# Performance work log

Measured on AMD Instinct MI355X. Metric: run time of the kernel, lower is better.

Reference implementation:

```python
import jax, jax.numpy as jnp
import numpy as np

B, T, I, H = 32768, 18, 2, 64  # batch, seq_len (forced by fc2 in_features=18), input_dim, hidden_dim


def setup_inputs() -> dict:
    key = jax.random.key(0)
    ks = jax.random.split(key, 13)
    s = 1.0 / np.sqrt(H)  # torch default GRU/Linear init scale
    return {
        "x": jax.random.normal(ks[0], (B, T, I), jnp.float32),
        "w_ih_f": jax.random.uniform(ks[1], (3 * H, I), jnp.float32, -s, s),
        "w_hh_f": jax.random.uniform(ks[2], (3 * H, H), jnp.float32, -s, s),
        "b_ih_f": jax.random.uniform(ks[3], (3 * H,), jnp.float32, -s, s),
        "b_hh_f": jax.random.uniform(ks[4], (3 * H,), jnp.float32, -s, s),
        "w_ih_b": jax.random.uniform(ks[5], (3 * H, I), jnp.float32, -s, s),
        "w_hh_b": jax.random.uniform(ks[6], (3 * H, H), jnp.float32, -s, s),
        "b_ih_b": jax.random.uniform(ks[7], (3 * H,), jnp.float32, -s, s),
        "b_hh_b": jax.random.uniform(ks[8], (3 * H,), jnp.float32, -s, s),
        "fc1_w": jax.random.uniform(ks[9], (24, 2 * H), jnp.float32, -s, s),
        "fc1_b": jax.random.uniform(ks[10], (24,), jnp.float32, -s, s),
        "fc2_w": jax.random.uniform(ks[11], (2, T), jnp.float32, -s, s),
        "fc2_b": jax.random.uniform(ks[12], (2,), jnp.float32, -s, s),
    }


def _gru_scan(x_proj, w_hh, b_hh):
    """x_proj: (T, B, 3H) precomputed input projections. Returns (T, B, H)."""
    h0 = jnp.zeros((x_proj.shape[1], w_hh.shape[1]), x_proj.dtype)

    def step(h, xp):
        gh = h @ w_hh.T + b_hh
        i_r, i_z, i_n = jnp.split(xp, 3, axis=-1)
        h_r, h_z, h_n = jnp.split(gh, 3, axis=-1)
        r = jax.nn.sigmoid(i_r + h_r)
        z = jax.nn.sigmoid(i_z + h_z)
        n = jnp.tanh(i_n + r * h_n)
        h_new = (1 - z) * n + z * h
        return h_new, h_new

    _, hs = jax.lax.scan(step, h0, x_proj)
    return hs


def reference(x, w_ih_f, w_hh_f, b_ih_f, b_hh_f,
              w_ih_b, w_hh_b, b_ih_b, b_hh_b,
              fc1_w, fc1_b, fc2_w, fc2_b):
    # precompute input-gate projections for both directions: (T, B, 3H)
    xp_f = jnp.einsum('bti,gi->tbg', x, w_ih_f) + b_ih_f
    xp_b = jnp.einsum('bti,gi->tbg', x[:, ::-1], w_ih_b) + b_ih_b
    hf = _gru_scan(xp_f, w_hh_f, b_hh_f)           # (T, B, H)
    hb = _gru_scan(xp_b, w_hh_b, b_hh_b)[::-1]     # (T, B, H), re-aligned to forward time
    out = jnp.concatenate([hf, hb], axis=-1).transpose(1, 0, 2)  # (B, T, 2H)
    out = out @ fc1_w.T + fc1_b                    # (B, T, 24)
    out = out.reshape(out.shape[0], 24, -1)        # (B, 24, T) raw row-major reshape, as in torch
    out = out @ fc2_w.T + fc2_b                    # (B, 24, 2)
    return out
```

## Files before the change

### kernel.cpp

```cpp
#include <hip/hip_runtime.h>

#define TT 18

typedef __attribute__((ext_vector_type(8))) short short8;
typedef __attribute__((ext_vector_type(4))) float float4_t;
typedef __attribute__((ext_vector_type(2))) float float2_t;
typedef __attribute__((ext_vector_type(2))) unsigned int uint2_t;

#if defined(__has_builtin)
#if __has_builtin(__builtin_amdgcn_exp2f)
#define FEXP2(x) __builtin_amdgcn_exp2f(x)
#else
#define FEXP2(x) exp2f(x)
#endif
#else
#define FEXP2(x) exp2f(x)
#endif

static __device__ __forceinline__ float frcp(float x){ return __builtin_amdgcn_rcpf(x); }
static __device__ __forceinline__ unsigned rne_bits(float f){
    unsigned u = __float_as_uint(f);
    return u + 0x7fffu + ((u >> 16) & 1u);
}
static __device__ __forceinline__ void bsplit(float f, unsigned &hi, unsigned &lo){
    unsigned rb = rne_bits(f);
    hi = rb >> 16;
    float fh = __uint_as_float(rb & 0xffff0000u);
    lo = rne_bits(f - fh) >> 16;
}
static __device__ __forceinline__ unsigned pack_hi16(unsigned hi_src, unsigned lo_src){
#if defined(__has_builtin)
#if __has_builtin(__builtin_amdgcn_perm)
    return __builtin_amdgcn_perm(hi_src, lo_src, 0x07060302u);
#else
    return (lo_src >> 16) | (hi_src & 0xffff0000u);
#endif
#else
    return (lo_src >> 16) | (hi_src & 0xffff0000u);
#endif
}

union U8 { short8 s; unsigned u[4]; };

#define MFMA16(A,B,C) __builtin_amdgcn_mfma_f32_16x16x32_bf16((A),(B),(C),0,0,0)

static __device__ __forceinline__ short8 make_b2f(float x0, float x1, bool q0){
    unsigned h0, l0, h1, l1;
    bsplit(x0, h0, l0);
    bsplit(x1, h1, l1);
    U8 B;
    B.u[0] = q0 ? (h0 | (l0 << 16)) : 0u;
    B.u[1] = q0 ? (h0 | (h1 << 16)) : 0u;
    B.u[2] = q0 ? (l1 | (h1 << 16)) : 0u;
    B.u[3] = q0 ? 0x3F803F80u : 0u;
    return B.s;
}

__global__ __launch_bounds__(256) void head_precompute(
    const float* __restrict__ fc1_w, const float* __restrict__ fc1_b,
    const float* __restrict__ fc2_w, const float* __restrict__ fc2_b,
    unsigned short* __restrict__ Bhi, unsigned short* __restrict__ Blo,
    float* __restrict__ Cvec)
{
    int idx = blockIdx.x * 256 + threadIdx.x;
    if (idx < 24 * 2 * 18 * 128) {
        int jg = idx & 127;
        int t  = (idx >> 7) % 18;
        int k  = (idx / 2304) & 1;
        int r  = idx / 4608;
        float acc = 0.f;
        for (int c = 0; c < 24; ++c) {
            int s = t * 24 + c - r * 18;
            if (s >= 0 && s < 18) acc += fc2_w[k * 18 + s] * fc1_w[c * 128 + jg];
        }
        unsigned hi, lo;
        bsplit(acc, hi, lo);
        Bhi[idx] = (unsigned short)hi;
        Blo[idx] = (unsigned short)lo;
    }
    if (idx < 48) {
        int k = idx & 1, r = idx >> 1;
        float acc = fc2_b[k];
        for (int s = 0; s < 18; ++s)
            acc += fc2_w[k * 18 + s] * fc1_b[(r * 18 + s) % 24];
        Cvec[idx] = acc;
    }
}

struct SMv {
    alignas(16) unsigned short hb[2][2][2][2048];
    float2_t x_s[32][18];
    float out_acc[2][32][49];
};

__global__ __launch_bounds__(512, 4) void gru_mfma(
    const float* __restrict__ x,
    const float* __restrict__ w_ih_f, const float* __restrict__ w_hh_f,
    const float* __restrict__ b_ih_f, const float* __restrict__ b_hh_f,
    const float* __restrict__ w_ih_b, const float* __restrict__ w_hh_b,
    const float* __restrict__ b_ih_b, const float* __restrict__ b_hh_b,
    const unsigned short* __restrict__ Bhi, const unsigned short* __restrict__ Blo,
    const float* __restrict__ Cvec, float* __restrict__ out)
{
    __shared__ SMv sm;
    const int tid  = threadIdx.x;
    const int lane = tid & 63;
    const int wave = tid >> 6;
    const int dir  = wave >> 2;
    const int jq   = wave & 3;
    const int col  = lane & 15;
    const int quad = lane >> 4;
    const int bb   = blockIdx.x * 32;
    const bool q0  = (quad == 0);

    const float* __restrict__ wih = dir ? w_ih_b : w_ih_f;
    const float* __restrict__ whh = dir ? w_hh_b : w_hh_f;
    const float* __restrict__ bih = dir ? b_ih_b : b_ih_f;
    const float* __restrict__ bhh = dir ? b_hh_b : b_hh_f;

    const float L1 = 1.4426950408889634f;
    const float L2 = 2.8853900817779268f;

    {
        unsigned* z = (unsigned*)&sm.hb[1][0][0][0];
        #pragma unroll
        for (int o = 0; o < 8; ++o) z[tid + o * 512] = 0u;
    }
    for (int o = tid; o < 2 * 32 * 49; o += 512) ((float*)sm.out_acc)[o] = 0.f;

    for (int p = tid; p < 32 * 18; p += 512) {
        int b = p / 18, t = p % 18;
        sm.x_s[b][t] = *(const float2_t*)(x + (size_t)(bb + b) * 36 + t * 2);
    }

    short8 wf[3][2];
    #pragma unroll
    for (int ty = 0; ty < 3; ++ty) {
        float sc = (ty == 2) ? L2 : L1;
        int g = ty * 64 + jq * 16 + col;
        #pragma unroll
        for (int c = 0; c < 2; ++c) {
            const float* p = whh + g * 64 + c * 32 + quad * 8;
            float4_t f0 = *(const float4_t*)p;
            float4_t f1 = *(const float4_t*)(p + 4);
            short8 s;
            #pragma unroll
            for (int e = 0; e < 8; ++e) {
                float f = (e < 4) ? f0[e] : f1[e - 4];
                s[e] = (short)(rne_bits(sc * f) >> 16);
            }
            wf[ty][c] = s;
        }
    }

    short8 c2[4];
    {
        int g0 = jq * 16 + col;
        #pragma unroll
        for (int ty = 0; ty < 2; ++ty) {
            int g = ty * 64 + g0;
            unsigned w0h, w0l, w1h, w1l, bh, bl;
            bsplit(L1 * wih[2 * g],     w0h, w0l);
            bsplit(L1 * wih[2 * g + 1], w1h, w1l);
            bsplit(L1 * (bih[g] + bhh[g]), bh, bl);
            U8 f;
            f.u[0] = q0 ? (w0h | (w0h << 16)) : 0u;
            f.u[1] = q0 ? (w0l | (w1h << 16)) : 0u;
            f.u[2] = q0 ? (w1h | (w1l << 16)) : 0u;
            f.u[3] = q0 ? (bh  | (bl  << 16)) : 0u;
            c2[ty] = f.s;
        }
        {
            unsigned bh, bl;
            bsplit(L2 * bhh[128 + g0], bh, bl);
            U8 f;
            f.u[0] = 0u; f.u[1] = 0u; f.u[2] = 0u;
            f.u[3] = q0 ? (bh | (bl << 16)) : 0u;
            c2[2] = f.s;
        }
        {
            int g = 128 + g0;
            unsigned w0h, w0l, w1h, w1l, bh, bl;
            bsplit(L2 * wih[2 * g],     w0h, w0l);
            bsplit(L2 * wih[2 * g + 1], w1h, w1l);
            bsplit(L2 * bih[g], bh, bl);
            U8 f;
            f.u[0] = q0 ? (w0h | (w0h << 16)) : 0u;
            f.u[1] = q0 ? (w0l | (w1h << 16)) : 0u;
            f.u[2] = q0 ? (w1h | (w1l << 16)) : 0u;
            f.u[3] = q0 ? (bh  | (bl  << 16)) : 0u;
            c2[3] = f.s;
        }
    }

    float hprev[8] = {0.f,0.f,0.f,0.f,0.f,0.f,0.f,0.f};

    __syncthreads();

    auto step = [&](int t, int pr, int pw) {
        const bool myturn = (t > 0) && (((t - 1) & 3) == jq);
        const int tx = dir ? (TT - 1 - t) : t;

        short8 h0c0 = *(const short8*)&sm.hb[pr][dir][0][quad * 256 + col * 8];
        short8 h0c1 = *(const short8*)&sm.hb[pr][dir][0][(4 + quad) * 256 + col * 8];
        short8 h1c0 = *(const short8*)&sm.hb[pr][dir][0][quad * 256 + (16 + col) * 8];
        short8 h1c1 = *(const short8*)&sm.hb[pr][dir][0][(4 + quad) * 256 + (16 + col) * 8];

        float2_t xv0 = sm.x_s[col][tx];
        float2_t xv1 = sm.x_s[16 + col][tx];
        short8 b2f0 = make_b2f(xv0[0], xv0[1], q0);
        short8 b2f1 = make_b2f(xv1[0], xv1[1], q0);

        short8 hA0, hA1, lA0, lA1, l0c0, l0c1, l1c0, l1c1;
        int base_h = 0;
        if (myturn) {
            int s  = t - 1;
            int ta = dir ? (TT - 1 - s) : s;
            base_h = 4 * (ta / 3) + ta % 3;
            int i  = col & 3;
            int rr = base_h + (i >> 1);
            int kk = i & 1;
            size_t boff = (size_t)((rr * 2 + kk) * TT + ta) * 128 + dir * 64 + quad * 8;
            hA0 = *(const short8*)(Bhi + boff);
            hA1 = *(const short8*)(Bhi + boff + 32);
            lA0 = *(const short8*)(Blo + boff);
            lA1 = *(const short8*)(Blo + boff + 32);
            l0c0 = *(const short8*)&sm.hb[pr][dir][1][quad * 256 + col * 8];
            l0c1 = *(const short8*)&sm.hb[pr][dir][1][(4 + quad) * 256 + col * 8];
            l1c0 = *(const short8*)&sm.hb[pr][dir][1][quad * 256 + (16 + col) * 8];
            l1c1 = *(const short8*)&sm.hb[pr][dir][1][(4 + quad) * 256 + (16 + col) * 8];
        }

        #pragma unroll
        for (int nt = 0; nt < 2; ++nt) {
            short8 hc0 = nt ? h1c0 : h0c0;
            short8 hc1 = nt ? h1c1 : h0c1;
            short8 b2f = nt ? b2f1 : b2f0;
            float4_t aR  = (float4_t){0.f,0.f,0.f,0.f};
            float4_t aZ  = (float4_t){0.f,0.f,0.f,0.f};
            float4_t aNH = (float4_t){0.f,0.f,0.f,0.f};
            float4_t aNX = (float4_t){0.f,0.f,0.f,0.f};
            aR  = MFMA16(wf[0][0], hc0, aR);
            aR  = MFMA16(wf[0][1], hc1, aR);
            aR  = MFMA16(c2[0],    b2f, aR);
            aZ  = MFMA16(wf[1][0], hc0, aZ);
            aZ  = MFMA16(wf[1][1], hc1, aZ);
            aZ  = MFMA16(c2[1],    b2f, aZ);
            aNH = MFMA16(wf[2][0], hc0, aNH);
            aNH = MFMA16(wf[2][1], hc1, aNH);
            aNH = MFMA16(c2[2],    b2f, aNH);
            aNX = MFMA16(c2[3],    b2f, aNX);

            unsigned rh[4], rl[4];
            #pragma unroll
            for (int reg = 0; reg < 4; ++reg) {
                float r = frcp(1.f + FEXP2(-aR[reg]));
                float z = frcp(1.f + FEXP2(-aZ[reg]));
                float a = fmaf(r, aNH[reg], aNX[reg]);
                float n = fmaf(2.f, frcp(1.f + FEXP2(-a)), -1.f);
                float hnew = fmaf(z, hprev[nt * 4 + reg] - n, n);
                hprev[nt * 4 + reg] = hnew;
                unsigned rb = rne_bits(hnew);
                rh[reg] = rb;
                rl[reg] = __float_as_uint(hnew - __uint_as_float(rb & 0xffff0000u));
            }
            int woff = (jq * 2 + (quad >> 1)) * 256 + (nt * 16 + col) * 8 + (quad & 1) * 4;
            uint2_t dh, dl;
            dh[0] = pack_hi16(rh[1], rh[0]);
            dh[1] = pack_hi16(rh[3], rh[2]);
            dl[0] = pack_hi16(rl[1], rl[0]);
            dl[1] = pack_hi16(rl[3], rl[2]);
            *(uint2_t*)&sm.hb[pw][dir][0][woff] = dh;
            *(uint2_t*)&sm.hb[pw][dir][1][woff] = dl;

            if (nt == 0 && myturn) {
                float4_t a0 = (float4_t){0.f,0.f,0.f,0.f};
                a0 = MFMA16(hA0, h0c0, a0);
                a0 = MFMA16(hA1, h0c1, a0);
                a0 = MFMA16(hA0, l0c0, a0);
                a0 = MFMA16(hA1, l0c1, a0);
                a0 = MFMA16(lA0, h0c0, a0);
                a0 = MFMA16(lA1, h0c1, a0);
                float4_t a1 = (float4_t){0.f,0.f,0.f,0.f};
                a1 = MFMA16(hA0, h1c0, a1);
                a1 = MFMA16(hA1, h1c1, a1);
                a1 = MFMA16(hA0, l1c0, a1);
                a1 = MFMA16(hA1, l1c1, a1);
                a1 = MFMA16(lA0, h1c0, a1);
                a1 = MFMA16(lA1, h1c1, a1);
                if (q0) {
                    #pragma unroll
                    for (int reg = 0; reg < 4; ++reg) {
                        int cell = (base_h + (reg >> 1)) * 2 + (reg & 1);
                        sm.out_acc[dir][col][cell]      += a0[reg];
                        sm.out_acc[dir][16 + col][cell] += a1[reg];
                    }
                }
            }
        }

        __syncthreads();
    };

    #pragma unroll 1
    for (int tt = 0; tt < 9; ++tt) {
        step(2 * tt,     1, 0);
        step(2 * tt + 1, 0, 1);
    }

    if (jq == ((TT - 1) & 3)) {
        int s  = TT - 1;
        int ta = dir ? 0 : s;
        int base_h = 4 * (ta / 3) + ta % 3;
        int i  = col & 3;
        int rr = base_h + (i >> 1);
        int kk = i & 1;
        size_t boff = (size_t)((rr * 2 + kk) * TT + ta) * 128 + dir * 64 + quad * 8;
        short8 hA0 = *(const short8*)(Bhi + boff);
        short8 hA1 = *(const short8*)(Bhi + boff + 32);
        short8 lA0 = *(const short8*)(Blo + boff);
        short8 lA1 = *(const short8*)(Blo + boff + 32);
        #pragma unroll
        for (int nt = 0; nt < 2; ++nt) {
            short8 hc0 = *(const short8*)&sm.hb[1][dir][0][quad * 256 + (nt * 16 + col) * 8];
            short8 hc1 = *(const short8*)&sm.hb[1][dir][0][(4 + quad) * 256 + (nt * 16 + col) * 8];
            short8 lc0 = *(const short8*)&sm.hb[1][dir][1][quad * 256 + (nt * 16 + col) * 8];
            short8 lc1 = *(const short8*)&sm.hb[1][dir][1][(4 + quad) * 256 + (nt * 16 + col) * 8];
            float4_t acch = (float4_t){0.f,0.f,0.f,0.f};
            acch = MFMA16(hA0, hc0, acch);
            acch = MFMA16(hA1, hc1, acch);
            acch = MFMA16(hA0, lc0, acch);
            acch = MFMA16(hA1, lc1, acch);
            acch = MFMA16(lA0, hc0, acch);
            acch = MFMA16(lA1, hc1, acch);
            if (q0) {
                #pragma unroll
                for (int reg = 0; reg < 4; ++reg) {
                    int cell = (base_h + (reg >> 1)) * 2 + (reg & 1);
                    sm.out_acc[dir][nt * 16 + col][cell] += acch[reg];
                }
            }
        }
    }
    __syncthreads();

    #pragma unroll
    for (int rep = 0; rep < 3; ++rep) {
        int o = rep * 512 + tid;
        int b = o / 48, c = o % 48;
        out[(size_t)bb * 48 + o] = sm.out_acc[0][b][c] + sm.out_acc[1][b][c] + Cvec[c];
    }
}

extern "C" void kernel_launch(void* const* d_in, const int* in_sizes, int n_in,
                              void* d_out, int out_size, void* d_ws, size_t ws_size,
                              hipStream_t stream) {
    const float* x      = (const float*)d_in[0];
    const float* w_ih_f = (const float*)d_in[1];
    const float* w_hh_f = (const float*)d_in[2];
    const float* b_ih_f = (const float*)d_in[3];
    const float* b_hh_f = (const float*)d_in[4];
    const float* w_ih_b = (const float*)d_in[5];
    const float* w_hh_b = (const float*)d_in[6];
    const float* b_ih_b = (const float*)d_in[7];
    const float* b_hh_b = (const float*)d_in[8];
    const float* fc1_w  = (const float*)d_in[9];
    const float* fc1_b  = (const float*)d_in[10];
    const float* fc2_w  = (const float*)d_in[11];
    const float* fc2_b  = (const float*)d_in[12];
    float* out  = (float*)d_out;

    float*          Cvec = (float*)d_ws;
    unsigned short* Bhi  = (unsigned short*)((char*)d_ws + 256);
    unsigned short* Blo  = Bhi + 110592;

    head_precompute<<<432, 256, 0, stream>>>(fc1_w, fc1_b, fc2_w, fc2_b, Bhi, Blo, Cvec);
    gru_mfma<<<1024, 512, 0, stream>>>(x, w_ih_f, w_hh_f, b_ih_f, b_hh_f,
                                       w_ih_b, w_hh_b, b_ih_b, b_hh_b,
                                       Bhi, Blo, Cvec, out);
}
```

Before: 181.4 us.

## Precompute x bf16 splits in LDS, prefetch head weights, raise occupancy bound

```diff
diff --git a/kernel.cpp b/kernel.cpp
--- a/kernel.cpp
+++ b/kernel.cpp
@@ -43,18 +43,6 @@
 union U8 { short8 s; unsigned u[4]; };
 
 #define MFMA16(A,B,C) __builtin_amdgcn_mfma_f32_16x16x32_bf16((A),(B),(C),0,0,0)
-
-static __device__ __forceinline__ short8 make_b2f(float x0, float x1, bool q0){
-    unsigned h0, l0, h1, l1;
-    bsplit(x0, h0, l0);
-    bsplit(x1, h1, l1);
-    U8 B;
-    B.u[0] = q0 ? (h0 | (l0 << 16)) : 0u;
-    B.u[1] = q0 ? (h0 | (h1 << 16)) : 0u;
-    B.u[2] = q0 ? (l1 | (h1 << 16)) : 0u;
-    B.u[3] = q0 ? 0x3F803F80u : 0u;
-    return B.s;
-}
 
 __global__ __launch_bounds__(256) void head_precompute(
     const float* __restrict__ fc1_w, const float* __restrict__ fc1_b,
@@ -89,11 +77,11 @@
 
 struct SMv {
     alignas(16) unsigned short hb[2][2][2][2048];
-    float2_t x_s[32][18];
+    unsigned int b2[32][18][3];
     float out_acc[2][32][49];
 };
 
-__global__ __launch_bounds__(512, 4) void gru_mfma(
+__global__ __launch_bounds__(512, 6) void gru_mfma(
     const float* __restrict__ x,
     const float* __restrict__ w_ih_f, const float* __restrict__ w_hh_f,
     const float* __restrict__ b_ih_f, const float* __restrict__ b_hh_f,
@@ -130,7 +118,13 @@
 
     for (int p = tid; p < 32 * 18; p += 512) {
         int b = p / 18, t = p % 18;
-        sm.x_s[b][t] = *(const float2_t*)(x + (size_t)(bb + b) * 36 + t * 2);
+        float2_t xv = *(const float2_t*)(x + (size_t)(bb + b) * 36 + t * 2);
+        unsigned h0, l0, h1, l1;
+        bsplit(xv[0], h0, l0);
+        bsplit(xv[1], h1, l1);
+        sm.b2[b][t][0] = h0 | (l0 << 16);
+        sm.b2[b][t][1] = h0 | (h1 << 16);
+        sm.b2[b][t][2] = l1 | (h1 << 16);
     }
 
     short8 wf[3][2];
@@ -193,6 +187,25 @@
         }
     }
 
+    U8 B0, B1;
+    B0.u[0] = 0u; B0.u[1] = 0u; B0.u[2] = 0u;
+    B0.u[3] = q0 ? 0x3F803F80u : 0u;
+    B1 = B0;
+
+    short8 hA0, hA1, lA0, lA1;
+    int s_pf = jq;
+    {
+        int ta = dir ? (TT - 1 - s_pf) : s_pf;
+        int i  = col & 3;
+        int rr = 4 * (ta / 3) + ta % 3 + (i >> 1);
+        int kk = i & 1;
+        size_t boff = (size_t)((rr * 2 + kk) * TT + ta) * 128 + dir * 64 + quad * 8;
+        hA0 = *(const short8*)(Bhi + boff);
+        hA1 = *(const short8*)(Bhi + boff + 32);
+        lA0 = *(const short8*)(Blo + boff);
+        lA1 = *(const short8*)(Blo + boff + 32);
+    }
+
     float hprev[8] = {0.f,0.f,0.f,0.f,0.f,0.f,0.f,0.f};
 
     __syncthreads();
@@ -206,25 +219,18 @@
         short8 h1c0 = *(const short8*)&sm.hb[pr][dir][0][quad * 256 + (16 + col) * 8];
         short8 h1c1 = *(const short8*)&sm.hb[pr][dir][0][(4 + quad) * 256 + (16 + col) * 8];
 
-        float2_t xv0 = sm.x_s[col][tx];
-        float2_t xv1 = sm.x_s[16 + col][tx];
-        short8 b2f0 = make_b2f(xv0[0], xv0[1], q0);
-        short8 b2f1 = make_b2f(xv1[0], xv1[1], q0);
-
-        short8 hA0, hA1, lA0, lA1, l0c0, l0c1, l1c0, l1c1;
+        if (q0) {
+            const unsigned* p0 = &sm.b2[col][tx][0];
+            const unsigned* p1 = &sm.b2[16 + col][tx][0];
+            B0.u[0] = p0[0]; B0.u[1] = p0[1]; B0.u[2] = p0[2];
+            B1.u[0] = p1[0]; B1.u[1] = p1[1]; B1.u[2] = p1[2];
+        }
+
+        short8 l0c0, l0c1, l1c0, l1c1;
         int base_h = 0;
         if (myturn) {
-            int s  = t - 1;
-            int ta = dir ? (TT - 1 - s) : s;
+            int ta = dir ? (TT - 1 - s_pf) : s_pf;
             base_h = 4 * (ta / 3) + ta % 3;
-            int i  = col & 3;
-            int rr = base_h + (i >> 1);
-            int kk = i & 1;
-            size_t boff = (size_t)((rr * 2 + kk) * TT + ta) * 128 + dir * 64 + quad * 8;
-            hA0 = *(const short8*)(Bhi + boff);
-            hA1 = *(const short8*)(Bhi + boff + 32);
-            lA0 = *(const short8*)(Blo + boff);
-            lA1 = *(const short8*)(Blo + boff + 32);
             l0c0 = *(const short8*)&sm.hb[pr][dir][1][quad * 256 + col * 8];
             l0c1 = *(const short8*)&sm.hb[pr][dir][1][(4 + quad) * 256 + col * 8];
             l1c0 = *(const short8*)&sm.hb[pr][dir][1][quad * 256 + (16 + col) * 8];
@@ -235,7 +241,7 @@
         for (int nt = 0; nt < 2; ++nt) {
             short8 hc0 = nt ? h1c0 : h0c0;
             short8 hc1 = nt ? h1c1 : h0c1;
-            short8 b2f = nt ? b2f1 : b2f0;
+            short8 b2f = nt ? B1.s : B0.s;
             float4_t aR  = (float4_t){0.f,0.f,0.f,0.f};
             float4_t aZ  = (float4_t){0.f,0.f,0.f,0.f};
             float4_t aNH = (float4_t){0.f,0.f,0.f,0.f};
@@ -299,6 +305,21 @@
             }
         }
 
+        if (myturn) {
+            s_pf += 4;
+            if (s_pf < TT) {
+                int ta = dir ? (TT - 1 - s_pf) : s_pf;
+                int i  = col & 3;
+                int rr = 4 * (ta / 3) + ta % 3 + (i >> 1);
+                int kk = i & 1;
+                size_t boff = (size_t)((rr * 2 + kk) * TT + ta) * 128 + dir * 64 + quad * 8;
+                hA0 = *(const short8*)(Bhi + boff);
+                hA1 = *(const short8*)(Bhi + boff + 32);
+                lA0 = *(const short8*)(Blo + boff);
+                lA1 = *(const short8*)(Blo + boff + 32);
+            }
+        }
+
         __syncthreads();
     };
 
@@ -309,17 +330,8 @@
     }
 
     if (jq == ((TT - 1) & 3)) {
-        int s  = TT - 1;
-        int ta = dir ? 0 : s;
+        int ta = dir ? 0 : (TT - 1);
         int base_h = 4 * (ta / 3) + ta % 3;
-        int i  = col & 3;
-        int rr = base_h + (i >> 1);
-        int kk = i & 1;
-        size_t boff = (size_t)((rr * 2 + kk) * TT + ta) * 128 + dir * 64 + quad * 8;
-        short8 hA0 = *(const short8*)(Bhi + boff);
-        short8 hA1 = *(const short8*)(Bhi + boff + 32);
-        short8 lA0 = *(const short8*)(Blo + boff);
-        short8 lA1 = *(const short8*)(Blo + boff + 32);
         #pragma unroll
         for (int nt = 0; nt < 2; ++nt) {
             short8 hc0 = *(const short8*)&sm.hb[1][dir][0][quad * 256 + (nt * 16 + col) * 8];
```

New measurement: 601.1 us. +231.4%, slower.

## Split GRU directions into separate 256-thread blocks and sum partial outputs

Applied to the files above, without the earlier changes.

```diff
diff --git a/kernel.cpp b/kernel.cpp
--- a/kernel.cpp
+++ b/kernel.cpp
@@ -87,30 +87,30 @@
     }
 }
 
-struct SMv {
-    alignas(16) unsigned short hb[2][2][2][2048];
+struct SMs {
+    alignas(16) unsigned short hb[2][2][2048];
     float2_t x_s[32][18];
-    float out_acc[2][32][49];
+    float out_acc[48][32];
 };
 
-__global__ __launch_bounds__(512, 4) void gru_mfma(
+__global__ __launch_bounds__(256, 4) void gru_mfma(
     const float* __restrict__ x,
     const float* __restrict__ w_ih_f, const float* __restrict__ w_hh_f,
     const float* __restrict__ b_ih_f, const float* __restrict__ b_hh_f,
     const float* __restrict__ w_ih_b, const float* __restrict__ w_hh_b,
     const float* __restrict__ b_ih_b, const float* __restrict__ b_hh_b,
     const unsigned short* __restrict__ Bhi, const unsigned short* __restrict__ Blo,
-    const float* __restrict__ Cvec, float* __restrict__ out)
+    const float* __restrict__ Cvec, float* __restrict__ part1,
+    float* __restrict__ out)
 {
-    __shared__ SMv sm;
+    __shared__ SMs sm;
     const int tid  = threadIdx.x;
     const int lane = tid & 63;
-    const int wave = tid >> 6;
-    const int dir  = wave >> 2;
-    const int jq   = wave & 3;
+    const int jq   = tid >> 6;
+    const int dir  = blockIdx.x & 1;
+    const int bb   = (blockIdx.x >> 1) * 32;
     const int col  = lane & 15;
     const int quad = lane >> 4;
-    const int bb   = blockIdx.x * 32;
     const bool q0  = (quad == 0);
 
     const float* __restrict__ wih = dir ? w_ih_b : w_ih_f;
@@ -122,13 +122,13 @@
     const float L2 = 2.8853900817779268f;
 
     {
-        unsigned* z = (unsigned*)&sm.hb[1][0][0][0];
-        #pragma unroll
-        for (int o = 0; o < 8; ++o) z[tid + o * 512] = 0u;
-    }
-    for (int o = tid; o < 2 * 32 * 49; o += 512) ((float*)sm.out_acc)[o] = 0.f;
-
-    for (int p = tid; p < 32 * 18; p += 512) {
+        unsigned* z = (unsigned*)&sm.hb[1][0][0];
+        #pragma unroll
+        for (int o = 0; o < 8; ++o) z[tid + o * 256] = 0u;
+    }
+    for (int o = tid; o < 48 * 32; o += 256) ((float*)sm.out_acc)[o] = 0.f;
+
+    for (int p = tid; p < 32 * 18; p += 256) {
         int b = p / 18, t = p % 18;
         sm.x_s[b][t] = *(const float2_t*)(x + (size_t)(bb + b) * 36 + t * 2);
     }
@@ -201,10 +201,10 @@
         const bool myturn = (t > 0) && (((t - 1) & 3) == jq);
         const int tx = dir ? (TT - 1 - t) : t;
 
-        short8 h0c0 = *(const short8*)&sm.hb[pr][dir][0][quad * 256 + col * 8];
-        short8 h0c1 = *(const short8*)&sm.hb[pr][dir][0][(4 + quad) * 256 + col * 8];
-        short8 h1c0 = *(const short8*)&sm.hb[pr][dir][0][quad * 256 + (16 + col) * 8];
-        short8 h1c1 = *(const short8*)&sm.hb[pr][dir][0][(4 + quad) * 256 + (16 + col) * 8];
+        short8 h0c0 = *(const short8*)&sm.hb[pr][0][quad * 256 + col * 8];
+        short8 h0c1 = *(const short8*)&sm.hb[pr][0][(4 + quad) * 256 + col * 8];
+        short8 h1c0 = *(const short8*)&sm.hb[pr][0][quad * 256 + (16 + col) * 8];
+        short8 h1c1 = *(const short8*)&sm.hb[pr][0][(4 + quad) * 256 + (16 + col) * 8];
 
         float2_t xv0 = sm.x_s[col][tx];
         float2_t xv1 = sm.x_s[16 + col][tx];
@@ -225,10 +225,10 @@
             hA1 = *(const short8*)(Bhi + boff + 32);
             lA0 = *(const short8*)(Blo + boff);
             lA1 = *(const short8*)(Blo + boff + 32);
-            l0c0 = *(const short8*)&sm.hb[pr][dir][1][quad * 256 + col * 8];
-            l0c1 = *(const short8*)&sm.hb[pr][dir][1][(4 + quad) * 256 + col * 8];
-            l1c0 = *(const short8*)&sm.hb[pr][dir][1][quad * 256 + (16 + col) * 8];
-            l1c1 = *(const short8*)&sm.hb[pr][dir][1][(4 + quad) * 256 + (16 + col) * 8];
+            l0c0 = *(const short8*)&sm.hb[pr][1][quad * 256 + col * 8];
+            l0c1 = *(const short8*)&sm.hb[pr][1][(4 + quad) * 256 + col * 8];
+            l1c0 = *(const short8*)&sm.hb[pr][1][quad * 256 + (16 + col) * 8];
+            l1c1 = *(const short8*)&sm.hb[pr][1][(4 + quad) * 256 + (16 + col) * 8];
         }
 
         #pragma unroll
@@ -270,8 +270,8 @@
             dh[1] = pack_hi16(rh[3], rh[2]);
             dl[0] = pack_hi16(rl[1], rl[0]);
             dl[1] = pack_hi16(rl[3], rl[2]);
-            *(uint2_t*)&sm.hb[pw][dir][0][woff] = dh;
-            *(uint2_t*)&sm.hb[pw][dir][1][woff] = dl;
+            *(uint2_t*)&sm.hb[pw][0][woff] = dh;
+            *(uint2_t*)&sm.hb[pw][1][woff] = dl;
 
             if (nt == 0 && myturn) {
                 float4_t a0 = (float4_t){0.f,0.f,0.f,0.f};
@@ -292,8 +292,8 @@
                     #pragma unroll
                     for (int reg = 0; reg < 4; ++reg) {
                         int cell = (base_h + (reg >> 1)) * 2 + (reg & 1);
-                        sm.out_acc[dir][col][cell]      += a0[reg];
-                        sm.out_acc[dir][16 + col][cell] += a1[reg];
+                        sm.out_acc[cell][col]      += a0[reg];
+                        sm.out_acc[cell][16 + col] += a1[reg];
                     }
                 }
             }
@@ -309,8 +309,7 @@
     }
 
     if (jq == ((TT - 1) & 3)) {
-        int s  = TT - 1;
-        int ta = dir ? 0 : s;
+        int ta = dir ? 0 : (TT - 1);
         int base_h = 4 * (ta / 3) + ta % 3;
         int i  = col & 3;
         int rr = base_h + (i >> 1);
@@ -322,10 +321,10 @@
         short8 lA1 = *(const short8*)(Blo + boff + 32);
         #pragma unroll
         for (int nt = 0; nt < 2; ++nt) {
-            short8 hc0 = *(const short8*)&sm.hb[1][dir][0][quad * 256 + (nt * 16 + col) * 8];
-            short8 hc1 = *(const short8*)&sm.hb[1][dir][0][(4 + quad) * 256 + (nt * 16 + col) * 8];
-            short8 lc0 = *(const short8*)&sm.hb[1][dir][1][quad * 256 + (nt * 16 + col) * 8];
-            short8 lc1 = *(const short8*)&sm.hb[1][dir][1][(4 + quad) * 256 + (nt * 16 + col) * 8];
+            short8 hc0 = *(const short8*)&sm.hb[1][0][quad * 256 + (nt * 16 + col) * 8];
+            short8 hc1 = *(const short8*)&sm.hb[1][0][(4 + quad) * 256 + (nt * 16 + col) * 8];
+            short8 lc0 = *(const short8*)&sm.hb[1][1][quad * 256 + (nt * 16 + col) * 8];
+            short8 lc1 = *(const short8*)&sm.hb[1][1][(4 + quad) * 256 + (nt * 16 + col) * 8];
             float4_t acch = (float4_t){0.f,0.f,0.f,0.f};
             acch = MFMA16(hA0, hc0, acch);
             acch = MFMA16(hA1, hc1, acch);
@@ -337,19 +336,32 @@
                 #pragma unroll
                 for (int reg = 0; reg < 4; ++reg) {
                     int cell = (base_h + (reg >> 1)) * 2 + (reg & 1);
-                    sm.out_acc[dir][nt * 16 + col][cell] += acch[reg];
+                    sm.out_acc[cell][nt * 16 + col] += acch[reg];
                 }
             }
         }
     }
     __syncthreads();
 
+    float* __restrict__ dst = dir ? (part1 + (size_t)bb * 48) : (out + (size_t)bb * 48);
     #pragma unroll
-    for (int rep = 0; rep < 3; ++rep) {
-        int o = rep * 512 + tid;
+    for (int rep = 0; rep < 6; ++rep) {
+        int o = rep * 256 + tid;
         int b = o / 48, c = o % 48;
-        out[(size_t)bb * 48 + o] = sm.out_acc[0][b][c] + sm.out_acc[1][b][c] + Cvec[c];
-    }
+        float v = sm.out_acc[c][b];
+        if (!dir) v += Cvec[c];
+        dst[o] = v;
+    }
+}
+
+__global__ __launch_bounds__(256) void sum_out(
+    const float* __restrict__ p1, float* __restrict__ out)
+{
+    int i = (blockIdx.x * 256 + threadIdx.x) * 4;
+    float4_t a = *(const float4_t*)(out + i);
+    float4_t b = *(const float4_t*)(p1 + i);
+    a = a + b;
+    *(float4_t*)(out + i) = a;
 }
 
 extern "C" void kernel_launch(void* const* d_in, const int* in_sizes, int n_in,
@@ -373,9 +385,11 @@
     float*          Cvec = (float*)d_ws;
     unsigned short* Bhi  = (unsigned short*)((char*)d_ws + 256);
     unsigned short* Blo  = Bhi + 110592;
+    float*          part1 = (float*)((char*)d_ws + 442880);
 
     head_precompute<<<432, 256, 0, stream>>>(fc1_w, fc1_b, fc2_w, fc2_b, Bhi, Blo, Cvec);
-    gru_mfma<<<1024, 512, 0, stream>>>(x, w_ih_f, w_hh_f, b_ih_f, b_hh_f,
+    gru_mfma<<<2048, 256, 0, stream>>>(x, w_ih_f, w_hh_f, b_ih_f, b_hh_f,
                                        w_ih_b, w_hh_b, b_ih_b, b_hh_b,
-                                       Bhi, Blo, Cvec, out);
-}
+                                       Bhi, Blo, Cvec, part1, out);
+    sum_out<<<1536, 256, 0, stream>>>(part1, out);
+}
```

New measurement: 179.5 us. Within noise of the previous version (-1.0%).
